# Kernel tuning notes

Measured on AMD Instinct MI355X. Metric: run time of the kernel, lower is better.

The kernel has to match this reference:

```python
import jax, jax.numpy as jnp
import numpy as np

C_IN, C_OUT, K, DG, PAD = 256, 256, 3, 2, 1
EPS = 1e-5


def setup_inputs() -> dict:
    key = jax.random.key(0)
    k = jax.random.split(key, 8)
    B, H, W = 4, 64, 64
    x = jax.random.normal(k[0], (B, C_IN, H, W), jnp.float32)
    # offset/mask conv (DCNv2 pack): 3 * dg * k * k output channels
    w_off = jax.random.normal(k[1], (3 * DG * K * K, C_IN, K, K), jnp.float32) * 0.01
    b_off = jnp.zeros((3 * DG * K * K,), jnp.float32)
    # main deformable conv weight
    w = jax.random.normal(k[2], (C_OUT, C_IN, K, K), jnp.float32) * (1.0 / np.sqrt(C_IN * K * K))
    b = jnp.zeros((C_OUT,), jnp.float32)
    # BatchNorm (eval mode: running stats)
    gamma = jnp.ones((C_OUT,), jnp.float32)
    beta = jnp.zeros((C_OUT,), jnp.float32)
    running_mean = jax.random.normal(k[3], (C_OUT,), jnp.float32) * 0.1
    running_var = jax.random.uniform(k[4], (C_OUT,), jnp.float32, 0.5, 1.5)
    return dict(x=x, w_off=w_off, b_off=b_off, w=w, b=b, gamma=gamma, beta=beta,
                running_mean=running_mean, running_var=running_var)


def _conv2d_same(x, w, b):
    y = jax.lax.conv_general_dilated(x, w, (1, 1), 'SAME',
                                     dimension_numbers=('NCHW', 'OIHW', 'NCHW'))
    return y + b[None, :, None, None]


def _deform_conv(x, w_off, b_off, w, b):
    B, C, H, W = x.shape
    K2 = K * K
    Cg = C // DG
    # offsets + modulation mask from internal conv (DCNv2 pack)
    om = _conv2d_same(x, w_off, b_off)            # [B, 3*DG*K2, H, W]
    o1, o2, m = jnp.split(om, 3, axis=1)
    mask = jax.nn.sigmoid(m).reshape(B, DG, 1, K2, H * W)
    off_y = o1.reshape(B, DG, K2, H, W)
    off_x = o2.reshape(B, DG, K2, H, W)
    # base sampling grid: output pixel + kernel tap - pad
    ki = jnp.arange(K)
    ky = (jnp.repeat(ki, K) - PAD).astype(jnp.float32)   # [K2]
    kx = (jnp.tile(ki, K) - PAD).astype(jnp.float32)     # [K2]
    py = off_y + ky[:, None, None] + jnp.arange(H, dtype=jnp.float32)[None, :, None]
    px = off_x + kx[:, None, None] + jnp.arange(W, dtype=jnp.float32)[None, None, :]
    y0 = jnp.floor(py)
    x0 = jnp.floor(px)
    ly = (py - y0).reshape(B, DG, 1, K2, H * W)
    lx = (px - x0).reshape(B, DG, 1, K2, H * W)
    y0i = y0.astype(jnp.int32)
    x0i = x0.astype(jnp.int32)
    xg = x.reshape(B, DG, Cg, H * W)

    def gather(yi, xi):
        # zero-padded bilinear corner gather, per deformable group
        valid = (yi >= 0) & (yi < H) & (xi >= 0) & (xi < W)
        lin = jnp.clip(yi, 0, H - 1) * W + jnp.clip(xi, 0, W - 1)
        v = jnp.take_along_axis(xg[:, :, :, None, :],
                                lin.reshape(B, DG, 1, K2, H * W), axis=-1)
        return v * valid.reshape(B, DG, 1, K2, H * W)

    val = (gather(y0i, x0i) * (1 - ly) * (1 - lx)
           + gather(y0i, x0i + 1) * (1 - ly) * lx
           + gather(y0i + 1, x0i) * ly * (1 - lx)
           + gather(y0i + 1, x0i + 1) * ly * lx)
    val = val * mask                               # [B, DG, Cg, K2, H*W]
    wr = w.reshape(C_OUT, DG, Cg, K2)
    out = jnp.einsum('bgckn,ogck->bon', val, wr).reshape(B, C_OUT, H, W)
    return out + b[None, :, None, None]


def reference(x, w_off, b_off, w, b, gamma, beta, running_mean, running_var):
    y = _deform_conv(x, w_off, b_off, w, b)
    inv = gamma / jnp.sqrt(running_var + EPS)
    y = (y - running_mean[None, :, None, None]) * inv[None, :, None, None] + beta[None, :, None, None]
    return jax.nn.relu(y)
```

## Files before the change

kernel.cpp:

```cpp
#include <hip/hip_runtime.h>
#include <math.h>

typedef __bf16 bf16x8 __attribute__((ext_vector_type(8)));
typedef float  f32x4  __attribute__((ext_vector_type(4)));
typedef int    i32x4  __attribute__((ext_vector_type(4)));

#define MFMA16(a, b, c) __builtin_amdgcn_mfma_f32_16x16x32_bf16((a), (b), (c), 0, 0, 0)

#define ATIDX(r, c) ((r) * 128 + (((c) ^ ((r) & 7)) * 8))

__global__ __launch_bounds__(256) void setup_kernel(
    const float* __restrict__ x, const float* __restrict__ w,
    const float* __restrict__ w_off, const float* __restrict__ bconv,
    const float* __restrict__ gamma, const float* __restrict__ beta,
    const float* __restrict__ mean, const float* __restrict__ var,
    __bf16* __restrict__ xT, __bf16* __restrict__ wFragD,
    __bf16* __restrict__ wFragO, float* __restrict__ sc,
    float* __restrict__ sh) {
  __shared__ float ws[16 * 128 * 9];
  int t = threadIdx.x;
  if (blockIdx.x < 1024) {
    int b = blockIdx.x >> 8, y = (blockIdx.x >> 2) & 63, cc = blockIdx.x & 3;
    for (int i = t; i < 4096; i += 256) {
      int cl = i >> 6, xc = i & 63;
      ws[cl * 65 + xc] = x[(((size_t)b * 256 + cc * 64 + cl) * 64 + y) * 64 + xc];
    }
    __syncthreads();
    for (int i = t; i < 4096; i += 256) {
      int xc = i >> 6, cl = i & 63;
      xT[(((size_t)b * 64 + y) * 64 + xc) * 256 + cc * 64 + cl] =
          (__bf16)ws[cl * 65 + xc];
    }
    return;
  }
  if (blockIdx.x < 1056) {
    int id = blockIdx.x - 1024;
    int g = id >> 4, ocb = id & 15;
    for (int i = t; i < 18432; i += 256) {
      int oc_l = i / 1152, rem = i % 1152;
      ws[oc_l * 1152 + rem] = w[(size_t)(ocb * 16 + oc_l) * 2304 + g * 1152 + rem];
    }
    __syncthreads();
    for (int i = t; i < 18432; i += 256) {
      int j = i & 7, lane8 = (i >> 3) & 63, kc = (i >> 9) & 3, ktap = i >> 11;
      int klocal = (lane8 >> 4) * 8 + j;
      int oc_l = lane8 & 15, ci_l = kc * 32 + klocal;
      float v = ws[oc_l * 1152 + ci_l * 9 + ktap];
      int gk = g * 9 + ktap;
      wFragD[((size_t)(gk * 4 + kc) * 16 + ocb) * 512 + (i & 511)] = (__bf16)v;
    }
    return;
  }
  {
    int id2 = blockIdx.x - 1056;
    int ocb = id2 >> 1, h = id2 & 1;
    for (int i = t; i < 18432; i += 256) {
      int oc_l = i / 1152, rem = i % 1152;
      int oc = ocb * 16 + oc_l;
      ws[oc_l * 1152 + rem] =
          (oc < 54) ? w_off[(size_t)oc * 2304 + h * 1152 + rem] : 0.f;
    }
    __syncthreads();
    for (int i = t; i < 18432; i += 256) {
      int j = i & 7, lane8 = (i >> 3) & 63, kcl = (i >> 9) & 3, ktap = i >> 11;
      int klocal = (lane8 >> 4) * 8 + j;
      int oc_l = lane8 & 15, ci_l = kcl * 32 + klocal;
      int kc = h * 4 + kcl;
      float v = ws[oc_l * 1152 + ci_l * 9 + ktap];
      wFragO[((size_t)(ktap * 8 + kc) * 4 + ocb) * 512 + (i & 511)] = (__bf16)v;
    }
    if (id2 == 0 && t < 256) {
      float s = gamma[t] * rsqrtf(var[t] + 1e-5f);
      sc[t] = s;
      sh[t] = (bconv[t] - mean[t]) * s + beta[t];
    }
  }
}

struct PhaseC {
  f32x4 swgtv[18 * 64];
  i32x4 slinv[18 * 64];
  __bf16 atile[2][64 * 128];
};
union FusedLDS {
  __bf16 rowbuf[3 * 66 * 256];
  PhaseC c;
};

__global__ __launch_bounds__(1024) void fused_kernel(
    const __bf16* __restrict__ xT, const __bf16* __restrict__ wFragD,
    const __bf16* __restrict__ wFragO, const float* __restrict__ b_off,
    const float* __restrict__ sc, const float* __restrict__ sh,
    float* __restrict__ out) {
  __shared__ __attribute__((aligned(16))) FusedLDS U;
  __shared__ float omrow[54 * 64];
  int t = threadIdx.x;
  int b = blockIdx.x >> 6, y = blockIdx.x & 63;
  int lane = t & 63, wv = t >> 6;
  int l15 = lane & 15, quad = lane >> 4;
  const __bf16* xTb = xT + (size_t)b * 64 * 64 * 256;
  bf16x8 z8;
  #pragma unroll
  for (int e = 0; e < 8; ++e) z8[e] = (__bf16)0.f;

  for (int i = t; i < 3 * 66 * 32; i += 1024) {
    int c = i & 31, px66 = (i >> 5) % 66, dy = i / 2112;
    int y2 = y + dy - 1, x2 = px66 - 1;
    bf16x8 v = z8;
    if (y2 >= 0 && y2 < 64 && x2 >= 0 && x2 < 64)
      v = *(const bf16x8*)(xTb + ((size_t)y2 * 64 + x2) * 256 + c * 8);
    *(bf16x8*)&U.rowbuf[dy * 16896 + px66 * 256 + ((c ^ (px66 & 7)) * 8)] = v;
  }
  __syncthreads();

  {
    int mq = wv & 3, ocq = wv >> 2;
    f32x4 acc0 = {0.f, 0.f, 0.f, 0.f};
    for (int tap = 0; tap < 9; ++tap) {
      int dy = tap / 3, dxs = tap % 3;
      const __bf16* bb = wFragO + ((size_t)(tap * 8) * 4 + ocq) * 512 + lane * 8;
      bf16x8 Bf[8];
      #pragma unroll
      for (int kc = 0; kc < 8; ++kc)
        Bf[kc] = *(const bf16x8*)(bb + (size_t)kc * 4 * 512);
      int p0 = mq * 16 + l15 + dxs;
      const __bf16* rb = U.rowbuf + dy * 16896;
      #pragma unroll
      for (int kc = 0; kc < 8; ++kc) {
        int c = kc * 4 + quad;
        bf16x8 a0 = *(const bf16x8*)&rb[p0 * 256 + ((c ^ (p0 & 7)) * 8)];
        acc0 = MFMA16(a0, Bf[kc], acc0);
      }
    }
    int oc = ocq * 16 + l15;
    if (oc < 54) {
      float bo = b_off[oc];
      f32x4 r = {acc0.x + bo, acc0.y + bo, acc0.z + bo, acc0.w + bo};
      *(f32x4*)&omrow[oc * 64 + mq * 16 + quad * 4] = r;
    }
  }
  __syncthreads();

  for (int i = t; i < 18 * 64; i += 1024) {
    int gk = i >> 6, p = i & 63;
    int k = gk % 9;
    float oy = omrow[gk * 64 + p];
    float ox = omrow[(18 + gk) * 64 + p];
    float mz = omrow[(36 + gk) * 64 + p];
    float mv = 1.f / (1.f + expf(-mz));
    float py  = (float)(y + (k / 3) - 1) + oy;
    float pxf = (float)(p + (k % 3) - 1) + ox;
    float y0f = floorf(py), x0f = floorf(pxf);
    int y0 = (int)y0f, x0 = (int)x0f;
    float ly = py - y0f, lx = pxf - x0f;
    int y1 = y0 + 1, x1 = x0 + 1;
    bool vy0 = (y0 >= 0) && (y0 < 64), vy1 = (y1 >= 0) && (y1 < 64);
    bool vx0 = (x0 >= 0) && (x0 < 64), vx1 = (x1 >= 0) && (x1 < 64);
    int cy0 = min(max(y0, 0), 63), cy1 = min(max(y1, 0), 63);
    int cx0 = min(max(x0, 0), 63), cx1 = min(max(x1, 0), 63);
    f32x4 sv;
    sv.x = (vy0 && vx0) ? (1.f - ly) * (1.f - lx) * mv : 0.f;
    sv.y = (vy0 && vx1) ? (1.f - ly) * lx * mv : 0.f;
    sv.z = (vy1 && vx0) ? ly * (1.f - lx) * mv : 0.f;
    sv.w = (vy1 && vx1) ? ly * lx * mv : 0.f;
    i32x4 lv;
    lv.x = (cy0 * 64 + cx0) * 256;
    lv.y = (cy0 * 64 + cx1) * 256;
    lv.z = (cy1 * 64 + cx0) * 256;
    lv.w = (cy1 * 64 + cx1) * 256;
    U.c.swgtv[i] = sv;
    U.c.slinv[i] = lv;
  }
  __syncthreads();

  {
    int p = t >> 4, c16 = t & 15;
    const __bf16* xg = xTb + c16 * 8;
    f32x4 sv = U.c.swgtv[p];
    i32x4 lv = U.c.slinv[p];
    bf16x8 c0 = *(const bf16x8*)(xg + lv.x);
    bf16x8 c1 = *(const bf16x8*)(xg + lv.y);
    bf16x8 c2 = *(const bf16x8*)(xg + lv.z);
    bf16x8 c3 = *(const bf16x8*)(xg + lv.w);
    bf16x8 o;
    #pragma unroll
    for (int e = 0; e < 8; ++e)
      o[e] = (__bf16)(sv.x * (float)c0[e] + sv.y * (float)c1[e]
                    + sv.z * (float)c2[e] + sv.w * (float)c3[e]);
    *(bf16x8*)&U.c.atile[0][ATIDX(p, c16)] = o;
  }

  f32x4 acc[4][2];
  #pragma unroll
  for (int fm = 0; fm < 4; ++fm) {
    acc[fm][0] = (f32x4){0.f, 0.f, 0.f, 0.f};
    acc[fm][1] = (f32x4){0.f, 0.f, 0.f, 0.f};
  }
  int nq = wv - 8;
  bf16x8 bn0, bn1;
  if (wv >= 8) {
    const __bf16* bb = wFragD + ((size_t)nq * 2) * 512 + lane * 8;
    bn0 = *(const bf16x8*)bb;
    bn1 = *(const bf16x8*)(bb + 512);
  }
  __syncthreads();

  for (int gk = 0; gk < 18; ++gk) {
    if (wv < 8) {
      if (gk < 17) {
        int gn = gk + 1;
        int c16 = t & 15, p = t >> 4;
        const __bf16* xg = xTb + (gn / 9) * 128 + c16 * 8;
        __bf16* dst = U.c.atile[(gk + 1) & 1];
        #pragma unroll
        for (int half = 0; half < 2; ++half) {
          int pp = p + half * 32;
          f32x4 sv = U.c.swgtv[gn * 64 + pp];
          i32x4 lv = U.c.slinv[gn * 64 + pp];
          bf16x8 c0 = *(const bf16x8*)(xg + lv.x);
          bf16x8 c1 = *(const bf16x8*)(xg + lv.y);
          bf16x8 c2 = *(const bf16x8*)(xg + lv.z);
          bf16x8 c3 = *(const bf16x8*)(xg + lv.w);
          bf16x8 o;
          #pragma unroll
          for (int e = 0; e < 8; ++e)
            o[e] = (__bf16)(sv.x * (float)c0[e] + sv.y * (float)c1[e]
                          + sv.z * (float)c2[e] + sv.w * (float)c3[e]);
          *(bf16x8*)&dst[ATIDX(pp, c16)] = o;
        }
      }
    } else {
      const __bf16* at = U.c.atile[gk & 1];
      #pragma unroll
      for (int kc = 0; kc < 4; ++kc) {
        bf16x8 b0 = bn0, b1 = bn1;
        int nidx = gk * 4 + kc + 1;
        if (nidx < 72) {
          const __bf16* bb = wFragD + ((size_t)nidx * 16 + nq * 2) * 512 + lane * 8;
          bn0 = *(const bf16x8*)bb;
          bn1 = *(const bf16x8*)(bb + 512);
        }
        #pragma unroll
        for (int fm = 0; fm < 4; ++fm) {
          bf16x8 a = *(const bf16x8*)&at[ATIDX(fm * 16 + l15, kc * 4 + quad)];
          acc[fm][0] = MFMA16(a, b0, acc[fm][0]);
          acc[fm][1] = MFMA16(a, b1, acc[fm][1]);
        }
      }
    }
    __syncthreads();
  }

  if (wv >= 8) {
    #pragma unroll
    for (int fm = 0; fm < 4; ++fm) {
      #pragma unroll
      for (int fn = 0; fn < 2; ++fn) {
        int oc = nq * 32 + fn * 16 + l15;
        float s = sc[oc], h = sh[oc];
        f32x4 v = acc[fm][fn];
        f32x4 r = {fmaxf(v.x * s + h, 0.f), fmaxf(v.y * s + h, 0.f),
                   fmaxf(v.z * s + h, 0.f), fmaxf(v.w * s + h, 0.f)};
        int pxs = fm * 16 + quad * 4;
        *(f32x4*)(out + (((size_t)b * 256 + oc) * 64 + y) * 64 + pxs) = r;
      }
    }
  }
}

extern "C" void kernel_launch(void* const* d_in, const int* in_sizes, int n_in,
                              void* d_out, int out_size, void* d_ws, size_t ws_size,
                              hipStream_t stream) {
  const float* x     = (const float*)d_in[0];
  const float* w_off = (const float*)d_in[1];
  const float* b_off = (const float*)d_in[2];
  const float* w     = (const float*)d_in[3];
  const float* bconv = (const float*)d_in[4];
  const float* gamma = (const float*)d_in[5];
  const float* beta  = (const float*)d_in[6];
  const float* rmean = (const float*)d_in[7];
  const float* rvar  = (const float*)d_in[8];
  float* out = (float*)d_out;

  __bf16* xT     = (__bf16*)d_ws;
  __bf16* wFragD = (__bf16*)((char*)d_ws + 8388608);
  __bf16* wFragO = (__bf16*)((char*)d_ws + 9568256);
  float*  sc     = (float*)((char*)d_ws + 9863168);
  float*  sh     = (float*)((char*)d_ws + 9864192);

  setup_kernel<<<1064, 256, 0, stream>>>(
      x, w, w_off, bconv, gamma, beta, rmean, rvar, xT, wFragD, wFragO, sc, sh);
  fused_kernel<<<4 * 64, 1024, 0, stream>>>(xT, wFragD, wFragO, b_off, sc, sh, out);
}
```

Baseline: 156.2 us.

## Spread weight repacking over many threads and reuse B fragments in offset conv

```diff
diff --git a/kernel.cpp b/kernel.cpp
--- a/kernel.cpp
+++ b/kernel.cpp
@@ -17,63 +17,44 @@
     __bf16* __restrict__ xT, __bf16* __restrict__ wFragD,
     __bf16* __restrict__ wFragO, float* __restrict__ sc,
     float* __restrict__ sh) {
-  __shared__ float ws[16 * 128 * 9];
+  __shared__ float xs[64][65];
   int t = threadIdx.x;
   if (blockIdx.x < 1024) {
     int b = blockIdx.x >> 8, y = (blockIdx.x >> 2) & 63, cc = blockIdx.x & 3;
     for (int i = t; i < 4096; i += 256) {
       int cl = i >> 6, xc = i & 63;
-      ws[cl * 65 + xc] = x[(((size_t)b * 256 + cc * 64 + cl) * 64 + y) * 64 + xc];
+      xs[cl][xc] = x[(((size_t)b * 256 + cc * 64 + cl) * 64 + y) * 64 + xc];
     }
     __syncthreads();
     for (int i = t; i < 4096; i += 256) {
       int xc = i >> 6, cl = i & 63;
-      xT[(((size_t)b * 64 + y) * 64 + xc) * 256 + cc * 64 + cl] =
-          (__bf16)ws[cl * 65 + xc];
+      xT[(((size_t)b * 64 + y) * 64 + xc) * 256 + cc * 64 + cl] = (__bf16)xs[cl][xc];
     }
     return;
   }
-  if (blockIdx.x < 1056) {
-    int id = blockIdx.x - 1024;
-    int g = id >> 4, ocb = id & 15;
-    for (int i = t; i < 18432; i += 256) {
-      int oc_l = i / 1152, rem = i % 1152;
-      ws[oc_l * 1152 + rem] = w[(size_t)(ocb * 16 + oc_l) * 2304 + g * 1152 + rem];
-    }
-    __syncthreads();
-    for (int i = t; i < 18432; i += 256) {
-      int j = i & 7, lane8 = (i >> 3) & 63, kc = (i >> 9) & 3, ktap = i >> 11;
-      int klocal = (lane8 >> 4) * 8 + j;
-      int oc_l = lane8 & 15, ci_l = kc * 32 + klocal;
-      float v = ws[oc_l * 1152 + ci_l * 9 + ktap];
-      int gk = g * 9 + ktap;
-      wFragD[((size_t)(gk * 4 + kc) * 16 + ocb) * 512 + (i & 511)] = (__bf16)v;
-    }
-    return;
-  }
-  {
-    int id2 = blockIdx.x - 1056;
-    int ocb = id2 >> 1, h = id2 & 1;
-    for (int i = t; i < 18432; i += 256) {
-      int oc_l = i / 1152, rem = i % 1152;
-      int oc = ocb * 16 + oc_l;
-      ws[oc_l * 1152 + rem] =
-          (oc < 54) ? w_off[(size_t)oc * 2304 + h * 1152 + rem] : 0.f;
-    }
-    __syncthreads();
-    for (int i = t; i < 18432; i += 256) {
-      int j = i & 7, lane8 = (i >> 3) & 63, kcl = (i >> 9) & 3, ktap = i >> 11;
-      int klocal = (lane8 >> 4) * 8 + j;
-      int oc_l = lane8 & 15, ci_l = kcl * 32 + klocal;
-      int kc = h * 4 + kcl;
-      float v = ws[oc_l * 1152 + ci_l * 9 + ktap];
-      wFragO[((size_t)(ktap * 8 + kc) * 4 + ocb) * 512 + (i & 511)] = (__bf16)v;
-    }
-    if (id2 == 0 && t < 256) {
-      float s = gamma[t] * rsqrtf(var[t] + 1e-5f);
-      sc[t] = s;
-      sh[t] = (bconv[t] - mean[t]) * s + beta[t];
-    }
+  int i = (blockIdx.x - 1024) * 256 + t;
+  if (i < 589824) {
+    int j = i & 7, lane = (i >> 3) & 63, ocb = (i >> 9) & 15;
+    int kc = (i >> 13) & 3, gk = i >> 15;
+    int klocal = (lane >> 4) * 8 + j;
+    int oc = ocb * 16 + (lane & 15);
+    int c = kc * 32 + klocal;
+    int g = gk / 9, ktap = gk % 9;
+    wFragD[i] = (__bf16)w[((size_t)oc * 256 + g * 128 + c) * 9 + ktap];
+  } else {
+    int i2 = i - 589824;
+    int j = i2 & 7, lane = (i2 >> 3) & 63, ocb = (i2 >> 9) & 3;
+    int kc = (i2 >> 11) & 7, tap = i2 >> 14;
+    int klocal = (lane >> 4) * 8 + j;
+    int oc = ocb * 16 + (lane & 15);
+    int ci = kc * 32 + klocal;
+    wFragO[i2] = (oc < 54) ? (__bf16)w_off[((size_t)oc * 256 + ci) * 9 + tap]
+                           : (__bf16)0.f;
+  }
+  if (i < 256) {
+    float s = gamma[i] * rsqrtf(var[i] + 1e-5f);
+    sc[i] = s;
+    sh[i] = (bconv[i] - mean[i]) * s + beta[i];
   }
 }
 
@@ -113,30 +94,36 @@
   }
   __syncthreads();
 
-  {
-    int mq = wv & 3, ocq = wv >> 2;
-    f32x4 acc0 = {0.f, 0.f, 0.f, 0.f};
+  if (wv < 4) {
+    int ocq = wv;
+    f32x4 acc4[4];
+    #pragma unroll
+    for (int fm = 0; fm < 4; ++fm) acc4[fm] = (f32x4){0.f, 0.f, 0.f, 0.f};
     for (int tap = 0; tap < 9; ++tap) {
       int dy = tap / 3, dxs = tap % 3;
       const __bf16* bb = wFragO + ((size_t)(tap * 8) * 4 + ocq) * 512 + lane * 8;
-      bf16x8 Bf[8];
-      #pragma unroll
-      for (int kc = 0; kc < 8; ++kc)
-        Bf[kc] = *(const bf16x8*)(bb + (size_t)kc * 4 * 512);
-      int p0 = mq * 16 + l15 + dxs;
       const __bf16* rb = U.rowbuf + dy * 16896;
       #pragma unroll
       for (int kc = 0; kc < 8; ++kc) {
+        bf16x8 Bf = *(const bf16x8*)(bb + (size_t)kc * 4 * 512);
         int c = kc * 4 + quad;
-        bf16x8 a0 = *(const bf16x8*)&rb[p0 * 256 + ((c ^ (p0 & 7)) * 8)];
-        acc0 = MFMA16(a0, Bf[kc], acc0);
+        #pragma unroll
+        for (int fm = 0; fm < 4; ++fm) {
+          int p0 = fm * 16 + l15 + dxs;
+          bf16x8 a0 = *(const bf16x8*)&rb[p0 * 256 + ((c ^ (p0 & 7)) * 8)];
+          acc4[fm] = MFMA16(a0, Bf, acc4[fm]);
+        }
       }
     }
     int oc = ocq * 16 + l15;
     if (oc < 54) {
       float bo = b_off[oc];
-      f32x4 r = {acc0.x + bo, acc0.y + bo, acc0.z + bo, acc0.w + bo};
-      *(f32x4*)&omrow[oc * 64 + mq * 16 + quad * 4] = r;
+      #pragma unroll
+      for (int fm = 0; fm < 4; ++fm) {
+        f32x4 r = {acc4[fm].x + bo, acc4[fm].y + bo,
+                   acc4[fm].z + bo, acc4[fm].w + bo};
+        *(f32x4*)&omrow[oc * 64 + fm * 16 + quad * 4] = r;
+      }
     }
   }
   __syncthreads();
@@ -288,7 +275,7 @@
   float*  sc     = (float*)((char*)d_ws + 9863168);
   float*  sh     = (float*)((char*)d_ws + 9864192);
 
-  setup_kernel<<<1064, 256, 0, stream>>>(
+  setup_kernel<<<1024 + 2880, 256, 0, stream>>>(
       x, w, w_off, bconv, gamma, beta, rmean, rvar, xT, wFragD, wFragO, sc, sh);
   fused_kernel<<<4 * 64, 1024, 0, stream>>>(xT, wFragD, wFragO, b_off, sc, sh, out);
 }
```

Result: faster. 131.9 us (-15.6%).
